# Kernel tuning notes

Hardware: AMD Instinct MI355X
Metric: run time of the kernel (lower is better)

## Reference

```python
import jax, jax.numpy as jnp
import numpy as np
from jax import lax

DN = ('NCDHW', 'OIDHW', 'NCDHW')

def conv3d(x, w, b=None):
    y = lax.conv_general_dilated(x, w, window_strides=(1, 1, 1), padding='SAME', dimension_numbers=DN)
    if b is not None:
        y = y + b[None, :, None, None, None]
    return y

def adaptive_conv(x, w):
    # x: [B,C,D,H,W]; w: [B,27,D,H,W] per-voxel 3x3x3 kernel weights
    B, C, D, H, W = x.shape
    xp = jnp.pad(x, ((0, 0), (0, 0), (1, 1), (1, 1), (1, 1)))
    out = jnp.zeros_like(x)
    idx = 0
    for i in range(3):
        for j in range(3):
            for k in range(3):
                out = out + xp[:, :, i:i + D, j:j + H, k:k + W] * w[:, idx][:, None]
                idx += 1
    return out

def setup_inputs() -> dict:
    key = jax.random.key(0)
    k1, k2, k3 = jax.random.split(key, 3)
    B, C, D, H, W = 1, 8, 128, 128, 128
    x = jax.random.normal(k1, (B, C, D, H, W), dtype=jnp.float32)
    w1 = jax.random.normal(k2, (8, 8, 3, 3, 3), dtype=jnp.float32) * 0.1
    b1 = jnp.zeros((8,), dtype=jnp.float32)
    w2 = jax.random.normal(k3, (27, 8, 3, 3, 3), dtype=jnp.float32) * 0.1
    return {"x": x, "w1": w1, "b1": b1, "w2": w2}

def reference(x, w1, b1, w2):
    # adaptive_block: per-voxel 27-tap weights from a small conv stack
    h = jax.nn.relu(conv3d(x, w1, b1))
    w = conv3d(h, w2)  # [B,27,D,H,W]
    # F.normalize(w, dim=1, p=1)
    n = jnp.sum(jnp.abs(w), axis=1, keepdims=True)
    w = w / jnp.maximum(n, 1e-12)
    out = x
    for _ in range(3):
        out = adaptive_conv(out, w)
    return out
```

## Files before the change

kernel.cpp:

```cpp
#include <hip/hip_runtime.h>
#include <hip/hip_bf16.h>

constexpr int HW2 = 16384;
constexpr int DHW = 2097152;

constexpr int PKG = 13;
constexpr int XT  = 130;

typedef short bf16x8 __attribute__((ext_vector_type(8)));
typedef float f32x4  __attribute__((ext_vector_type(4)));

__device__ inline unsigned short f2b(float f) {
  __hip_bfloat16 h = __float2bfloat16(f);
  return *(unsigned short*)&h;
}
__device__ inline float b2f(unsigned short u) {
  __hip_bfloat16 h = *(__hip_bfloat16*)&u;
  return __bfloat162float(h);
}

__global__ __launch_bounds__(256) void k_prep(
    const float* __restrict__ w1, const float* __restrict__ w2,
    unsigned short* __restrict__ Wpack2, unsigned short* __restrict__ Wpack1,
    float* __restrict__ g_ti, float* __restrict__ g_xi) {
  int i = blockIdx.x * 256 + threadIdx.x;
  if (i < 9216) {
    int j = i & 7;
    int lane = (i >> 3) & 63;
    int Mt = (i >> 9) & 1;
    int g2 = i >> 10;
    int s = g2 % 3, dx = g2 / 3;
    int oc = Mt * 16 + (lane & 15);
    int kr = s * 32 + (lane >> 4) * 8 + j;
    int ci = kr & 7, g = kr >> 3;
    float w = 0.f;
    if (oc < 27 && (g & 3) < 3) {
      int dzr = g >> 2, dyr = g & 3;
      w = w2[(oc * 8 + ci) * 27 + dzr * 9 + dyr * 3 + dx];
    }
    Wpack2[i] = f2b(w);
  }
  int jj = i - 9216;
  if (jj >= 0 && jj < 4608) {
    int j = jj & 7;
    int lane = (jj >> 3) & 63;
    int g2 = jj >> 9;
    int s = g2 % 3, dx = g2 / 3;
    int oc = lane & 15;
    int kr = s * 32 + (lane >> 4) * 8 + j;
    int ci = kr & 7, g = kr >> 3;
    float w = 0.f;
    if (oc < 8 && (g & 3) < 3) {
      int dzr = g >> 2, dyr = g & 3;
      w = w1[(oc * 8 + ci) * 27 + dzr * 9 + dyr * 3 + dx];
    }
    Wpack1[jj] = f2b(w);
  }
  int gg = i - 13824;
  if (gg >= 0 && gg < 32) {
    float* p = (gg < 8)  ? (g_ti - 8 + gg)
             : (gg < 16) ? (g_ti + (size_t)8 * DHW + (gg - 8))
             : (gg < 24) ? (g_xi - 8 + (gg - 16))
                         : (g_xi + (size_t)8 * DHW + (gg - 24));
    *p = 0.f;
  }
}

__global__ __launch_bounds__(256) void k_xpose(
    const float* __restrict__ x, unsigned short* __restrict__ xb,
    float* __restrict__ xi) {
  int idx = blockIdx.x * 256 + threadIdx.x;
  float f[8];
  unsigned v[4];
#pragma unroll
  for (int p = 0; p < 4; ++p) {
    f[2 * p]     = x[(size_t)(2 * p) * DHW + idx];
    f[2 * p + 1] = x[(size_t)(2 * p + 1) * DHW + idx];
    unsigned lo = f2b(f[2 * p]);
    unsigned hi = f2b(f[2 * p + 1]);
    v[p] = lo | (hi << 16);
  }
  ((uint4*)xb)[idx] = make_uint4(v[0], v[1], v[2], v[3]);
  float4* xo = (float4*)(xi + (size_t)idx * 8);
  xo[0] = make_float4(f[0], f[1], f[2], f[3]);
  xo[1] = make_float4(f[4], f[5], f[6], f[7]);
}

#define STAGE_ROWS2(srcp)                                                  \
  {                                                                        \
    if (tid < 154) {                                                       \
      if (tid < 130) {                                                     \
        dst[tid * PKG + 12] = make_uint4(0u, 0u, 0u, 0u);                  \
      } else {                                                             \
        int k = tid - 130;                                                 \
        int sl = k >> 1, xih = (k & 1) ? 129 : 0;                          \
        dst[xih * PKG + sl] = make_uint4(0u, 0u, 0u, 0u);                  \
      }                                                                    \
    }                                                                      \
    const int gg = tid >> 7;                                               \
    const int xi_ = (tid & 127) + 1;                                       \
    const int xg_ = xi_ - 1;                                               \
    uint4 sv[6];                                                           \
    bool vld[6];                                                           \
    _Pragma("unroll")                                                      \
    for (int it = 0; it < 6; ++it) {                                       \
      const int g = gg + it * 2;                                           \
      const int dz = g >> 2, ry = g & 3;                                   \
      const int z = z0 + dz - 1, y = y0 + ry - 1;                          \
      vld[it] = ((unsigned)z < 128u) & ((unsigned)y < 128u);               \
      const int zz = vld[it] ? z : z0, yy = vld[it] ? y : y0;              \
      sv[it] = (srcp)[(zz * 128 + yy) * 128 + xg_];                        \
    }                                                                      \
    _Pragma("unroll")                                                      \
    for (int it = 0; it < 6; ++it) {                                       \
      const int g = gg + it * 2;                                           \
      uint4 v = vld[it] ? sv[it] : make_uint4(0u, 0u, 0u, 0u);             \
      dst[xi_ * PKG + g] = v;                                              \
    }                                                                      \
  }

__global__ __launch_bounds__(256, 3) void k_conv1m(
    const unsigned short* __restrict__ xb,
    const unsigned short* __restrict__ Wpack1,
    const float* __restrict__ b1, unsigned short* __restrict__ hb) {
  __shared__ __align__(16) unsigned short T[XT * PKG * 8];
  const int tid  = threadIdx.x;
  const int lane = tid & 63;
  const int wv   = tid >> 6;
  const int logical = (blockIdx.x & 7) * 1024 + (blockIdx.x >> 3);
  const int z0 = logical >> 6;
  const int y0 = (logical & 63) * 2;

  bf16x8 wf[3][3];
  {
    const bf16x8* wp = (const bf16x8*)Wpack1;
#pragma unroll
    for (int dx = 0; dx < 3; ++dx)
#pragma unroll
      for (int s = 0; s < 3; ++s)
        wf[dx][s] = wp[(dx * 3 + s) * 64 + lane];
  }

  const uint4* src = (const uint4*)xb;
  uint4* dst = (uint4*)T;
  STAGE_ROWS2(src);
  __syncthreads();

  f32x4 acc[2][2];
#pragma unroll
  for (int r = 0; r < 2; ++r)
#pragma unroll
    for (int nt = 0; nt < 2; ++nt) acc[r][nt] = (f32x4){0.f, 0.f, 0.f, 0.f};

  const int n = lane & 15;
  const int q = lane >> 4;
  const int xbase = wv * 32 + n;

#pragma unroll
  for (int dx = 0; dx < 3; ++dx) {
#pragma unroll
    for (int s = 0; s < 3; ++s) {
      bf16x8 bfr[2][2];
#pragma unroll
      for (int r = 0; r < 2; ++r)
#pragma unroll
        for (int nt = 0; nt < 2; ++nt) {
          int off = ((xbase + nt * 16 + dx) * PKG + (s * 4 + q + r)) * 8;
          bfr[r][nt] = *(const bf16x8*)&T[off];
        }
#pragma unroll
      for (int r = 0; r < 2; ++r)
#pragma unroll
        for (int nt = 0; nt < 2; ++nt)
          acc[r][nt] = __builtin_amdgcn_mfma_f32_16x16x32_bf16(
              wf[dx][s], bfr[r][nt], acc[r][nt], 0, 0, 0);
    }
  }

  if (q < 2) {
#pragma unroll
    for (int r = 0; r < 2; ++r) {
      const int voxrow = (z0 * 128 + y0 + r) * 128;
#pragma unroll
      for (int nt = 0; nt < 2; ++nt) {
        const int vox = voxrow + wv * 32 + nt * 16 + n;
        ushort4 o;
        o.x = f2b(fmaxf(acc[r][nt][0] + b1[q * 4 + 0], 0.f));
        o.y = f2b(fmaxf(acc[r][nt][1] + b1[q * 4 + 1], 0.f));
        o.z = f2b(fmaxf(acc[r][nt][2] + b1[q * 4 + 2], 0.f));
        o.w = f2b(fmaxf(acc[r][nt][3] + b1[q * 4 + 3], 0.f));
        *(ushort4*)(hb + (size_t)vox * 8 + q * 4) = o;
      }
    }
  }
}

__global__ __launch_bounds__(256, 2) void k_conv2(
    const unsigned short* __restrict__ hb,
    const unsigned short* __restrict__ Wpack2,
    unsigned short* __restrict__ wn) {
  __shared__ __align__(16) unsigned short T[XT * PKG * 8];
  const int tid  = threadIdx.x;
  const int lane = tid & 63;
  const int wv   = tid >> 6;
  const int logical = (blockIdx.x & 7) * 1024 + (blockIdx.x >> 3);
  const int z0 = logical >> 6;
  const int y0 = (logical & 63) * 2;

  bf16x8 wf[3][3][2];
  {
    const bf16x8* wp = (const bf16x8*)Wpack2;
#pragma unroll
    for (int dx = 0; dx < 3; ++dx)
#pragma unroll
      for (int s = 0; s < 3; ++s)
#pragma unroll
        for (int mt = 0; mt < 2; ++mt)
          wf[dx][s][mt] = wp[((dx * 3 + s) * 2 + mt) * 64 + lane];
  }

  const uint4* src = (const uint4*)hb;
  uint4* dst = (uint4*)T;
  STAGE_ROWS2(src);
  __syncthreads();

  f32x4 acc[2][2][2];
#pragma unroll
  for (int r = 0; r < 2; ++r)
#pragma unroll
    for (int nt = 0; nt < 2; ++nt)
#pragma unroll
      for (int mt = 0; mt < 2; ++mt)
        acc[r][nt][mt] = (f32x4){0.f, 0.f, 0.f, 0.f};

  const int n = lane & 15;
  const int q = lane >> 4;
  const int xbase = wv * 32 + n;

#pragma unroll
  for (int dx = 0; dx < 3; ++dx) {
#pragma unroll
    for (int s = 0; s < 3; ++s) {
      bf16x8 bfr[2][2];
#pragma unroll
      for (int r = 0; r < 2; ++r)
#pragma unroll
        for (int nt = 0; nt < 2; ++nt) {
          int off = ((xbase + nt * 16 + dx) * PKG + (s * 4 + q + r)) * 8;
          bfr[r][nt] = *(const bf16x8*)&T[off];
        }
#pragma unroll
      for (int r = 0; r < 2; ++r)
#pragma unroll
        for (int mt = 0; mt < 2; ++mt)
#pragma unroll
          for (int nt = 0; nt < 2; ++nt)
            acc[r][nt][mt] = __builtin_amdgcn_mfma_f32_16x16x32_bf16(
                wf[dx][s][mt], bfr[r][nt], acc[r][nt][mt], 0, 0, 0);
    }
  }

#pragma unroll
  for (int r = 0; r < 2; ++r) {
    const int voxrow = (z0 * 128 + y0 + r) * 128;
#pragma unroll
    for (int nt = 0; nt < 2; ++nt) {
      float ns = 0.f;
#pragma unroll
      for (int rr = 0; rr < 4; ++rr) ns += fabsf(acc[r][nt][0][rr]);
#pragma unroll
      for (int rr = 0; rr < 4; ++rr) {
        int oc = 16 + q * 4 + rr;
        ns += (oc < 27) ? fabsf(acc[r][nt][1][rr]) : 0.f;
      }
      ns += __shfl_xor(ns, 16);
      ns += __shfl_xor(ns, 32);
      float sc = 1.f / fmaxf(ns, 1e-12f);
      const int vox = voxrow + wv * 32 + nt * 16 + n;
#pragma unroll
      for (int rr = 0; rr < 4; ++rr) {
        int oc = q * 4 + rr;
        wn[(size_t)oc * DHW + vox] = f2b(acc[r][nt][0][rr] * sc);
      }
#pragma unroll
      for (int rr = 0; rr < 4; ++rr) {
        int oc = 16 + q * 4 + rr;
        if (oc < 27)
          wn[(size_t)oc * DHW + vox] = f2b(acc[r][nt][1][rr] * sc);
      }
    }
  }
}

__device__ inline int swzb(int off) { return off ^ (((off >> 7) & 7) << 4); }

template <int FINAL>
__global__ __launch_bounds__(256, 2) void k_adapt4(
    const float* __restrict__ in, const unsigned short* __restrict__ wn,
    float* __restrict__ out) {
  __shared__ __align__(16) char S[16 * 4224];
  const int tid = threadIdx.x;
  const int logical = (blockIdx.x & 7) * 512 + (blockIdx.x >> 3);
  const int ty = logical & 63, tz = logical >> 6;
  const int y0 = ty * 2, z0 = tz * 2;

  const int wv = tid >> 6, lane = tid & 63;
  const int zl = wv >> 1, yl = wv & 1;
  const int zout = z0 + zl, yout = y0 + yl;
  const int xg = lane * 2;
  const int vox0 = (zout * 128 + yout) * 128 + xg;

  uint4 stg[16];
#pragma unroll
  for (int c = 0; c < 16; ++c) {
    const int zs = min(max(z0 - 1 + (c >> 2), 0), 127);
    const int ys = min(max(y0 - 1 + (c & 3), 0), 127);
    stg[c] = ((const uint4*)(in + (size_t)(zs * 128 + ys) * 1024))[tid];
  }

  unsigned wnv[27];
#pragma unroll
  for (int k = 0; k < 27; ++k)
    wnv[k] = *(const unsigned*)(wn + (size_t)k * DHW + vox0);

  {
    const int off = swzb(32 + tid * 16);
#pragma unroll
    for (int c = 0; c < 16; ++c)
      *(uint4*)(S + c * 4224 + off) = stg[c];
  }
  if (tid < 64) {
    const int row = tid >> 2, part = tid & 3;
    const int off = (part < 2) ? part * 16 : (4128 + (part - 2) * 16);
    *(uint4*)(S + row * 4224 + swzb(off)) = make_uint4(0u, 0u, 0u, 0u);
  }
  __syncthreads();

  int soff[4][2];
#pragma unroll
  for (int p = 0; p < 4; ++p)
#pragma unroll
    for (int h = 0; h < 2; ++h)
      soff[p][h] = swzb((xg + p) * 32 + h * 16);

  f32x4 a0A = (f32x4){0.f, 0.f, 0.f, 0.f};
  f32x4 a0B = (f32x4){0.f, 0.f, 0.f, 0.f};
  f32x4 a1A = (f32x4){0.f, 0.f, 0.f, 0.f};
  f32x4 a1B = (f32x4){0.f, 0.f, 0.f, 0.f};

#pragma unroll
  for (int g = 0; g < 9; ++g) {
    const int dzp = g / 3, dyp = g % 3;
    const char* R = S + ((zl + dzp) * 4 + (yl + dyp)) * 4224;
    f32x4 W[4][2];
#pragma unroll
    for (int p = 0; p < 4; ++p)
#pragma unroll
      for (int h = 0; h < 2; ++h)
        W[p][h] = *(const f32x4*)(R + soff[p][h]);
    const bool val = ((unsigned)(zout + dzp - 1) < 128u) &
                     ((unsigned)(yout + dyp - 1) < 128u);
#pragma unroll
    for (int dxi = 0; dxi < 3; ++dxi) {
      const unsigned u = wnv[g * 3 + dxi];
      const float wl = val ? b2f((unsigned short)(u & 0xffffu)) : 0.f;
      const float wh = val ? b2f((unsigned short)(u >> 16)) : 0.f;
#pragma unroll
      for (int c = 0; c < 4; ++c) {
        a0A[c] = fmaf(W[dxi][0][c], wl, a0A[c]);
        a0B[c] = fmaf(W[dxi][1][c], wl, a0B[c]);
        a1A[c] = fmaf(W[dxi + 1][0][c], wh, a1A[c]);
        a1B[c] = fmaf(W[dxi + 1][1][c], wh, a1B[c]);
      }
    }
  }

  if (FINAL) {
#pragma unroll
    for (int c = 0; c < 4; ++c) {
      *(float2*)(out + (size_t)c * DHW + vox0) = make_float2(a0A[c], a1A[c]);
      *(float2*)(out + (size_t)(c + 4) * DHW + vox0) =
          make_float2(a0B[c], a1B[c]);
    }
  } else {
    f32x4* op = (f32x4*)(out + (size_t)vox0 * 8);
    op[0] = a0A;
    op[1] = a0B;
    op[2] = a1A;
    op[3] = a1B;
  }
}

extern "C" void kernel_launch(void* const* d_in, const int* in_sizes, int n_in,
                              void* d_out, int out_size, void* d_ws, size_t ws_size,
                              hipStream_t stream) {
  const float* x  = (const float*)d_in[0];
  const float* w1 = (const float*)d_in[1];
  const float* b1 = (const float*)d_in[2];
  const float* w2 = (const float*)d_in[3];
  float* out = (float*)d_out;

  char* ws = (char*)d_ws;
  unsigned short* xb = (unsigned short*)ws;
  unsigned short* hb = (unsigned short*)(ws + (size_t)8 * DHW * 2);
  float* ti = (float*)(ws + 256);
  unsigned short* wn = (unsigned short*)(ws + (size_t)16 * DHW * 2 + 4096);
  float* xi = (float*)(ws + (size_t)16 * DHW * 2 + 4096 +
                       (size_t)27 * DHW * 2 + 8192);
  unsigned short* Wpack2 =
      (unsigned short*)((char*)xi + (size_t)8 * DHW * 4 + 16384);
  unsigned short* Wpack1 = Wpack2 + 9216;

  dim3 blk(256);
  k_prep<<<55, blk, 0, stream>>>(w1, w2, Wpack2, Wpack1, ti, xi);
  k_xpose<<<DHW / 256, blk, 0, stream>>>(x, xb, xi);
  k_conv1m<<<128 * 64, blk, 0, stream>>>(xb, Wpack1, b1, hb);
  k_conv2<<<128 * 64, blk, 0, stream>>>(hb, Wpack2, wn);
  k_adapt4<0><<<64 * 64, blk, 0, stream>>>(xi, wn, ti);
  k_adapt4<0><<<64 * 64, blk, 0, stream>>>(ti, wn, xi);
  k_adapt4<1><<<64 * 64, blk, 0, stream>>>(xi, wn, out);
}
```

Baseline: 353.3 us.

## Make adaptive conv kernel persistent over 8 y-tiles with register-prefetch pipelining

```diff
diff --git a/kernel.cpp b/kernel.cpp
--- a/kernel.cpp
+++ b/kernel.cpp
@@ -294,100 +294,149 @@
 
 __device__ inline int swzb(int off) { return off ^ (((off >> 7) & 7) << 4); }
 
+#define AD_ISSUE_X(ty_)                                                   \
+  {                                                                       \
+    const int ys0_ = 2 * (ty_) - 1;                                       \
+    _Pragma("unroll")                                                     \
+    for (int c = 0; c < 16; ++c) {                                        \
+      const int ys_ = min(max(ys0_ + (c & 3), 0), 127);                   \
+      stg[c] =                                                            \
+          ((const uint4*)(in + (size_t)(zs4[c >> 2] * 128 + ys_) * 1024)) \
+              [tid];                                                      \
+    }                                                                     \
+  }
+
+#define AD_ISSUE_WN(W_, ty_)                                              \
+  {                                                                       \
+    const int vox_ = (zrow + 2 * (ty_) + yl) * 128 + xg;                  \
+    _Pragma("unroll")                                                     \
+    for (int k2 = 0; k2 < 27; ++k2)                                       \
+      W_[k2] = *(const unsigned*)(wn + (size_t)k2 * DHW + vox_);          \
+  }
+
+#define AD_DSW()                                                          \
+  {                                                                       \
+    _Pragma("unroll")                                                     \
+    for (int c = 0; c < 16; ++c)                                          \
+      *(uint4*)(S + c * 4224 + woff) = stg[c];                            \
+  }
+
+#define AD_COMPUTE(W_, ty_)                                               \
+  {                                                                       \
+    const int yout_ = 2 * (ty_) + yl;                                     \
+    const int vox0_ = (zrow + yout_) * 128 + xg;                          \
+    f32x4 a0A = (f32x4){0.f, 0.f, 0.f, 0.f};                              \
+    f32x4 a0B = (f32x4){0.f, 0.f, 0.f, 0.f};                              \
+    f32x4 a1A = (f32x4){0.f, 0.f, 0.f, 0.f};                              \
+    f32x4 a1B = (f32x4){0.f, 0.f, 0.f, 0.f};                              \
+    _Pragma("unroll")                                                     \
+    for (int g = 0; g < 9; ++g) {                                         \
+      const int dzp_ = g / 3, dyp_ = g % 3;                               \
+      const char* R_ = S + ((zl + dzp_) * 4 + (yl + dyp_)) * 4224;        \
+      f32x4 W4[4][2];                                                     \
+      _Pragma("unroll")                                                   \
+      for (int p = 0; p < 4; ++p)                                         \
+        _Pragma("unroll")                                                 \
+        for (int h = 0; h < 2; ++h)                                       \
+          W4[p][h] = *(const f32x4*)(R_ + soff[p][h]);                    \
+      const bool val_ =                                                   \
+          zok[dzp_] & ((unsigned)(yout_ + dyp_ - 1) < 128u);              \
+      _Pragma("unroll")                                                   \
+      for (int dxi = 0; dxi < 3; ++dxi) {                                 \
+        const unsigned u_ = W_[g * 3 + dxi];                              \
+        const float wl_ =                                                 \
+            val_ ? b2f((unsigned short)(u_ & 0xffffu)) : 0.f;             \
+        const float wh_ = val_ ? b2f((unsigned short)(u_ >> 16)) : 0.f;   \
+        _Pragma("unroll")                                                 \
+        for (int c = 0; c < 4; ++c) {                                     \
+          a0A[c] = fmaf(W4[dxi][0][c], wl_, a0A[c]);                      \
+          a0B[c] = fmaf(W4[dxi][1][c], wl_, a0B[c]);                      \
+          a1A[c] = fmaf(W4[dxi + 1][0][c], wh_, a1A[c]);                  \
+          a1B[c] = fmaf(W4[dxi + 1][1][c], wh_, a1B[c]);                  \
+        }                                                                 \
+      }                                                                   \
+    }                                                                     \
+    if (FINAL) {                                                          \
+      _Pragma("unroll")                                                   \
+      for (int c = 0; c < 4; ++c) {                                       \
+        *(float2*)(out + (size_t)c * DHW + vox0_) =                       \
+            make_float2(a0A[c], a1A[c]);                                  \
+        *(float2*)(out + (size_t)(c + 4) * DHW + vox0_) =                 \
+            make_float2(a0B[c], a1B[c]);                                  \
+      }                                                                   \
+    } else {                                                              \
+      f32x4* op_ = (f32x4*)(out + (size_t)vox0_ * 8);                     \
+      op_[0] = a0A;                                                       \
+      op_[1] = a0B;                                                       \
+      op_[2] = a1A;                                                       \
+      op_[3] = a1B;                                                       \
+    }                                                                     \
+  }
+
 template <int FINAL>
-__global__ __launch_bounds__(256, 2) void k_adapt4(
+__global__ __launch_bounds__(256, 2) void k_adapt5(
     const float* __restrict__ in, const unsigned short* __restrict__ wn,
     float* __restrict__ out) {
   __shared__ __align__(16) char S[16 * 4224];
   const int tid = threadIdx.x;
-  const int logical = (blockIdx.x & 7) * 512 + (blockIdx.x >> 3);
-  const int ty = logical & 63, tz = logical >> 6;
-  const int y0 = ty * 2, z0 = tz * 2;
-
   const int wv = tid >> 6, lane = tid & 63;
   const int zl = wv >> 1, yl = wv & 1;
-  const int zout = z0 + zl, yout = y0 + yl;
   const int xg = lane * 2;
-  const int vox0 = (zout * 128 + yout) * 128 + xg;
-
-  uint4 stg[16];
-#pragma unroll
-  for (int c = 0; c < 16; ++c) {
-    const int zs = min(max(z0 - 1 + (c >> 2), 0), 127);
-    const int ys = min(max(y0 - 1 + (c & 3), 0), 127);
-    stg[c] = ((const uint4*)(in + (size_t)(zs * 128 + ys) * 1024))[tid];
-  }
-
-  unsigned wnv[27];
-#pragma unroll
-  for (int k = 0; k < 27; ++k)
-    wnv[k] = *(const unsigned*)(wn + (size_t)k * DHW + vox0);
-
-  {
-    const int off = swzb(32 + tid * 16);
-#pragma unroll
-    for (int c = 0; c < 16; ++c)
-      *(uint4*)(S + c * 4224 + off) = stg[c];
-  }
+
+  const int logical_b = ((blockIdx.x & 7) << 6) + (blockIdx.x >> 3);
+  const int tz = logical_b >> 3;
+  const int ty0 = (logical_b & 7) * 8;
+
+  int zs4[4];
+#pragma unroll
+  for (int d = 0; d < 4; ++d) zs4[d] = min(max(2 * tz - 1 + d, 0), 127);
+  bool zok[3];
+#pragma unroll
+  for (int d = 0; d < 3; ++d)
+    zok[d] = (unsigned)(2 * tz + zl + d - 1) < 128u;
+  const int zrow = (2 * tz + zl) * 128;
+
+  const int woff = swzb(32 + tid * 16);
+  int soff[4][2];
+#pragma unroll
+  for (int p = 0; p < 4; ++p)
+#pragma unroll
+    for (int h = 0; h < 2; ++h)
+      soff[p][h] = swzb((xg + p) * 32 + h * 16);
+
   if (tid < 64) {
     const int row = tid >> 2, part = tid & 3;
     const int off = (part < 2) ? part * 16 : (4128 + (part - 2) * 16);
-    *(uint4*)(S + row * 4224 + swzb(off)) = make_uint4(0u, 0u, 0u, 0u);
-  }
+    *(uint4*)(S + row * 4224 + off) = make_uint4(0u, 0u, 0u, 0u);
+  }
+
+  uint4 stg[16];
+  unsigned wnA[27], wnB[27];
+
+  AD_ISSUE_X(ty0);
+  AD_ISSUE_WN(wnA, ty0);
+  AD_DSW();
   __syncthreads();
 
-  int soff[4][2];
-#pragma unroll
-  for (int p = 0; p < 4; ++p)
-#pragma unroll
-    for (int h = 0; h < 2; ++h)
-      soff[p][h] = swzb((xg + p) * 32 + h * 16);
-
-  f32x4 a0A = (f32x4){0.f, 0.f, 0.f, 0.f};
-  f32x4 a0B = (f32x4){0.f, 0.f, 0.f, 0.f};
-  f32x4 a1A = (f32x4){0.f, 0.f, 0.f, 0.f};
-  f32x4 a1B = (f32x4){0.f, 0.f, 0.f, 0.f};
-
-#pragma unroll
-  for (int g = 0; g < 9; ++g) {
-    const int dzp = g / 3, dyp = g % 3;
-    const char* R = S + ((zl + dzp) * 4 + (yl + dyp)) * 4224;
-    f32x4 W[4][2];
-#pragma unroll
-    for (int p = 0; p < 4; ++p)
-#pragma unroll
-      for (int h = 0; h < 2; ++h)
-        W[p][h] = *(const f32x4*)(R + soff[p][h]);
-    const bool val = ((unsigned)(zout + dzp - 1) < 128u) &
-                     ((unsigned)(yout + dyp - 1) < 128u);
-#pragma unroll
-    for (int dxi = 0; dxi < 3; ++dxi) {
-      const unsigned u = wnv[g * 3 + dxi];
-      const float wl = val ? b2f((unsigned short)(u & 0xffffu)) : 0.f;
-      const float wh = val ? b2f((unsigned short)(u >> 16)) : 0.f;
-#pragma unroll
-      for (int c = 0; c < 4; ++c) {
-        a0A[c] = fmaf(W[dxi][0][c], wl, a0A[c]);
-        a0B[c] = fmaf(W[dxi][1][c], wl, a0B[c]);
-        a1A[c] = fmaf(W[dxi + 1][0][c], wh, a1A[c]);
-        a1B[c] = fmaf(W[dxi + 1][1][c], wh, a1B[c]);
-      }
-    }
-  }
-
-  if (FINAL) {
-#pragma unroll
-    for (int c = 0; c < 4; ++c) {
-      *(float2*)(out + (size_t)c * DHW + vox0) = make_float2(a0A[c], a1A[c]);
-      *(float2*)(out + (size_t)(c + 4) * DHW + vox0) =
-          make_float2(a0B[c], a1B[c]);
-    }
-  } else {
-    f32x4* op = (f32x4*)(out + (size_t)vox0 * 8);
-    op[0] = a0A;
-    op[1] = a0B;
-    op[2] = a1A;
-    op[3] = a1B;
+#pragma unroll 1
+  for (int k = 0; k < 4; ++k) {
+    const int tyA = ty0 + 2 * k;
+    const int tyB = tyA + 1;
+    const int tyC = (k < 3) ? (tyA + 2) : tyB;
+
+    AD_ISSUE_X(tyB);
+    AD_ISSUE_WN(wnB, tyB);
+    AD_COMPUTE(wnA, tyA);
+    __syncthreads();
+    AD_DSW();
+    __syncthreads();
+
+    AD_ISSUE_X(tyC);
+    AD_ISSUE_WN(wnA, tyC);
+    AD_COMPUTE(wnB, tyB);
+    __syncthreads();
+    AD_DSW();
+    __syncthreads();
   }
 }
 
@@ -416,7 +465,7 @@
   k_xpose<<<DHW / 256, blk, 0, stream>>>(x, xb, xi);
   k_conv1m<<<128 * 64, blk, 0, stream>>>(xb, Wpack1, b1, hb);
   k_conv2<<<128 * 64, blk, 0, stream>>>(hb, Wpack2, wn);
-  k_adapt4<0><<<64 * 64, blk, 0, stream>>>(xi, wn, ti);
-  k_adapt4<0><<<64 * 64, blk, 0, stream>>>(ti, wn, xi);
-  k_adapt4<1><<<64 * 64, blk, 0, stream>>>(xi, wn, out);
-}
+  k_adapt5<0><<<512, blk, 0, stream>>>(xi, wn, ti);
+  k_adapt5<0><<<512, blk, 0, stream>>>(ti, wn, xi);
+  k_adapt5<1><<<512, blk, 0, stream>>>(xi, wn, out);
+}
```

Measured after the change: 820.5 us. 2.32x slower.

## Use one voxel per thread with 512-thread blocks in adaptive conv

Applied to the files above, without the earlier changes.

```diff
diff --git a/kernel.cpp b/kernel.cpp
--- a/kernel.cpp
+++ b/kernel.cpp
@@ -292,10 +292,12 @@
   }
 }
 
-__device__ inline int swzb(int off) { return off ^ (((off >> 7) & 7) << 4); }
+__device__ inline int swzb(int off) {
+  return off ^ ((((off >> 7) ^ (off >> 10)) & 7) << 4);
+}
 
 template <int FINAL>
-__global__ __launch_bounds__(256, 2) void k_adapt4(
+__global__ __launch_bounds__(512, 2) void k_adapt6(
     const float* __restrict__ in, const unsigned short* __restrict__ wn,
     float* __restrict__ out) {
   __shared__ __align__(16) char S[16 * 4224];
@@ -304,30 +306,34 @@
   const int ty = logical & 63, tz = logical >> 6;
   const int y0 = ty * 2, z0 = tz * 2;
 
-  const int wv = tid >> 6, lane = tid & 63;
-  const int zl = wv >> 1, yl = wv & 1;
+  const int r = tid >> 7;
+  const int zl = r >> 1, yl = r & 1;
+  const int x = tid & 127;
   const int zout = z0 + zl, yout = y0 + yl;
-  const int xg = lane * 2;
-  const int vox0 = (zout * 128 + yout) * 128 + xg;
-
-  uint4 stg[16];
-#pragma unroll
-  for (int c = 0; c < 16; ++c) {
-    const int zs = min(max(z0 - 1 + (c >> 2), 0), 127);
-    const int ys = min(max(y0 - 1 + (c & 3), 0), 127);
-    stg[c] = ((const uint4*)(in + (size_t)(zs * 128 + ys) * 1024))[tid];
-  }
-
-  unsigned wnv[27];
+  const int vox = (zout * 128 + yout) * 128 + x;
+
+  const int sh = tid >> 8;
+  const int spos = tid & 255;
+
+  uint4 stg[8];
+#pragma unroll
+  for (int c = 0; c < 8; ++c) {
+    const int row = sh * 8 + c;
+    const int zs = min(max(z0 - 1 + (row >> 2), 0), 127);
+    const int ys = min(max(y0 - 1 + (row & 3), 0), 127);
+    stg[c] = ((const uint4*)(in + (size_t)(zs * 128 + ys) * 1024))[spos];
+  }
+
+  unsigned short wnv[27];
 #pragma unroll
   for (int k = 0; k < 27; ++k)
-    wnv[k] = *(const unsigned*)(wn + (size_t)k * DHW + vox0);
+    wnv[k] = wn[(size_t)k * DHW + vox];
 
   {
-    const int off = swzb(32 + tid * 16);
-#pragma unroll
-    for (int c = 0; c < 16; ++c)
-      *(uint4*)(S + c * 4224 + off) = stg[c];
+    const int woff = swzb(32 + spos * 16);
+#pragma unroll
+    for (int c = 0; c < 8; ++c)
+      *(uint4*)(S + (sh * 8 + c) * 4224 + woff) = stg[c];
   }
   if (tid < 64) {
     const int row = tid >> 2, part = tid & 3;
@@ -336,58 +342,57 @@
   }
   __syncthreads();
 
-  int soff[4][2];
-#pragma unroll
-  for (int p = 0; p < 4; ++p)
+  int soff[3][2];
+#pragma unroll
+  for (int p = 0; p < 3; ++p)
 #pragma unroll
     for (int h = 0; h < 2; ++h)
-      soff[p][h] = swzb((xg + p) * 32 + h * 16);
-
-  f32x4 a0A = (f32x4){0.f, 0.f, 0.f, 0.f};
-  f32x4 a0B = (f32x4){0.f, 0.f, 0.f, 0.f};
-  f32x4 a1A = (f32x4){0.f, 0.f, 0.f, 0.f};
-  f32x4 a1B = (f32x4){0.f, 0.f, 0.f, 0.f};
-
+      soff[p][h] = swzb((x + p) * 32 + h * 16);
+
+  bool zok[3], yok[3];
+#pragma unroll
+  for (int d = 0; d < 3; ++d) {
+    zok[d] = (unsigned)(zout + d - 1) < 128u;
+    yok[d] = (unsigned)(yout + d - 1) < 128u;
+  }
+
+  f32x4 aA = (f32x4){0.f, 0.f, 0.f, 0.f};
+  f32x4 aB = (f32x4){0.f, 0.f, 0.f, 0.f};
+
+  __builtin_amdgcn_s_setprio(1);
 #pragma unroll
   for (int g = 0; g < 9; ++g) {
     const int dzp = g / 3, dyp = g % 3;
     const char* R = S + ((zl + dzp) * 4 + (yl + dyp)) * 4224;
-    f32x4 W[4][2];
-#pragma unroll
-    for (int p = 0; p < 4; ++p)
+    f32x4 W[3][2];
+#pragma unroll
+    for (int p = 0; p < 3; ++p)
 #pragma unroll
       for (int h = 0; h < 2; ++h)
         W[p][h] = *(const f32x4*)(R + soff[p][h]);
-    const bool val = ((unsigned)(zout + dzp - 1) < 128u) &
-                     ((unsigned)(yout + dyp - 1) < 128u);
+    const bool val = zok[dzp] & yok[dyp];
 #pragma unroll
     for (int dxi = 0; dxi < 3; ++dxi) {
-      const unsigned u = wnv[g * 3 + dxi];
-      const float wl = val ? b2f((unsigned short)(u & 0xffffu)) : 0.f;
-      const float wh = val ? b2f((unsigned short)(u >> 16)) : 0.f;
+      const float w = val ? b2f(wnv[g * 3 + dxi]) : 0.f;
 #pragma unroll
       for (int c = 0; c < 4; ++c) {
-        a0A[c] = fmaf(W[dxi][0][c], wl, a0A[c]);
-        a0B[c] = fmaf(W[dxi][1][c], wl, a0B[c]);
-        a1A[c] = fmaf(W[dxi + 1][0][c], wh, a1A[c]);
-        a1B[c] = fmaf(W[dxi + 1][1][c], wh, a1B[c]);
+        aA[c] = fmaf(W[dxi][0][c], w, aA[c]);
+        aB[c] = fmaf(W[dxi][1][c], w, aB[c]);
       }
     }
   }
+  __builtin_amdgcn_s_setprio(0);
 
   if (FINAL) {
 #pragma unroll
     for (int c = 0; c < 4; ++c) {
-      *(float2*)(out + (size_t)c * DHW + vox0) = make_float2(a0A[c], a1A[c]);
-      *(float2*)(out + (size_t)(c + 4) * DHW + vox0) =
-          make_float2(a0B[c], a1B[c]);
+      out[(size_t)c * DHW + vox] = aA[c];
+      out[(size_t)(c + 4) * DHW + vox] = aB[c];
     }
   } else {
-    f32x4* op = (f32x4*)(out + (size_t)vox0 * 8);
-    op[0] = a0A;
-    op[1] = a0B;
-    op[2] = a1A;
-    op[3] = a1B;
+    f32x4* op = (f32x4*)(out + (size_t)vox * 8);
+    op[0] = aA;
+    op[1] = aB;
   }
 }
 
@@ -412,11 +417,12 @@
   unsigned short* Wpack1 = Wpack2 + 9216;
 
   dim3 blk(256);
+  dim3 blk512(512);
   k_prep<<<55, blk, 0, stream>>>(w1, w2, Wpack2, Wpack1, ti, xi);
   k_xpose<<<DHW / 256, blk, 0, stream>>>(x, xb, xi);
   k_conv1m<<<128 * 64, blk, 0, stream>>>(xb, Wpack1, b1, hb);
   k_conv2<<<128 * 64, blk, 0, stream>>>(hb, Wpack2, wn);
-  k_adapt4<0><<<64 * 64, blk, 0, stream>>>(xi, wn, ti);
-  k_adapt4<0><<<64 * 64, blk, 0, stream>>>(ti, wn, xi);
-  k_adapt4<1><<<64 * 64, blk, 0, stream>>>(xi, wn, out);
-}
+  k_adapt6<0><<<64 * 64, blk512, 0, stream>>>(xi, wn, ti);
+  k_adapt6<0><<<64 * 64, blk512, 0, stream>>>(ti, wn, xi);
+  k_adapt6<1><<<64 * 64, blk512, 0, stream>>>(xi, wn, out);
+}
```

After: 359.6 us. Within noise of the previous version (+1.8%).

## Retile adaptive conv to 4x4x64 blocks with two y-outputs per thread

Applied to the files above, without the earlier changes.

```diff
diff --git a/kernel.cpp b/kernel.cpp
--- a/kernel.cpp
+++ b/kernel.cpp
@@ -292,102 +292,142 @@
   }
 }
 
-__device__ inline int swzb(int off) { return off ^ (((off >> 7) & 7) << 4); }
+constexpr int APITCH = 2112;
+__device__ inline int swz7(int off) { return off ^ (((off >> 7) & 7) << 4); }
 
 template <int FINAL>
-__global__ __launch_bounds__(256, 2) void k_adapt4(
+__global__ __launch_bounds__(256, 2) void k_adapt7(
     const float* __restrict__ in, const unsigned short* __restrict__ wn,
     float* __restrict__ out) {
-  __shared__ __align__(16) char S[16 * 4224];
+  __shared__ __align__(16) char S[36 * APITCH];
   const int tid = threadIdx.x;
-  const int logical = (blockIdx.x & 7) * 512 + (blockIdx.x >> 3);
-  const int ty = logical & 63, tz = logical >> 6;
-  const int y0 = ty * 2, z0 = tz * 2;
-
-  const int wv = tid >> 6, lane = tid & 63;
-  const int zl = wv >> 1, yl = wv & 1;
-  const int zout = z0 + zl, yout = y0 + yl;
-  const int xg = lane * 2;
-  const int vox0 = (zout * 128 + yout) * 128 + xg;
-
-  uint4 stg[16];
-#pragma unroll
-  for (int c = 0; c < 16; ++c) {
-    const int zs = min(max(z0 - 1 + (c >> 2), 0), 127);
-    const int ys = min(max(y0 - 1 + (c & 3), 0), 127);
-    stg[c] = ((const uint4*)(in + (size_t)(zs * 128 + ys) * 1024))[tid];
-  }
-
-  unsigned wnv[27];
-#pragma unroll
-  for (int k = 0; k < 27; ++k)
-    wnv[k] = *(const unsigned*)(wn + (size_t)k * DHW + vox0);
-
-  {
-    const int off = swzb(32 + tid * 16);
-#pragma unroll
-    for (int c = 0; c < 16; ++c)
-      *(uint4*)(S + c * 4224 + off) = stg[c];
-  }
-  if (tid < 64) {
-    const int row = tid >> 2, part = tid & 3;
-    const int off = (part < 2) ? part * 16 : (4128 + (part - 2) * 16);
-    *(uint4*)(S + row * 4224 + swzb(off)) = make_uint4(0u, 0u, 0u, 0u);
+  const int logical = (blockIdx.x & 7) * 256 + (blockIdx.x >> 3);
+  const int xh  = logical & 1;
+  const int typ = (logical >> 1) & 31;
+  const int tzp = logical >> 6;
+  const int x0 = xh * 64, y0 = typ * 4, z0 = tzp * 4;
+
+  const int xp = tid & 31;
+  const int yp = (tid >> 5) & 1;
+  const int zo = tid >> 6;
+
+  uint4 stg[19];
+#pragma unroll
+  for (int i = 0; i < 19; ++i) {
+    const int c = tid + 256 * i;
+    if (c < 4752) {
+      const int r = c / 132;
+      const int k = c - r * 132;
+      const int r6 = r / 6;
+      const int zs = min(max(z0 - 1 + r6, 0), 127);
+      const int ys = min(max(y0 - 1 + (r - r6 * 6), 0), 127);
+      const float* gp = in + (size_t)(zs * 128 + ys) * 1024 +
+                        (ptrdiff_t)((x0 - 1) * 8 + k * 4);
+      stg[i] = *(const uint4*)gp;
+    }
+  }
+#pragma unroll
+  for (int i = 0; i < 19; ++i) {
+    const int c = tid + 256 * i;
+    if (c < 4752) {
+      const int r = c / 132;
+      const int k = c - r * 132;
+      const bool halo = xh ? (k >= 130) : (k < 2);
+      const uint4 v = halo ? make_uint4(0u, 0u, 0u, 0u) : stg[i];
+      *(uint4*)(S + r * APITCH + swz7(k * 16)) = v;
+    }
   }
   __syncthreads();
 
+  const int Y = y0 + 2 * yp;
+  const int Z = z0 + zo;
+  bool zok[3];
+#pragma unroll
+  for (int d = 0; d < 3; ++d) zok[d] = (unsigned)(Z + d - 1) < 128u;
+  bool yok[2][3];
+#pragma unroll
+  for (int oy = 0; oy < 2; ++oy)
+#pragma unroll
+    for (int d = 0; d < 3; ++d)
+      yok[oy][d] = (unsigned)(Y + oy + d - 1) < 128u;
+
   int soff[4][2];
 #pragma unroll
-  for (int p = 0; p < 4; ++p)
+  for (int j = 0; j < 4; ++j)
 #pragma unroll
     for (int h = 0; h < 2; ++h)
-      soff[p][h] = swzb((xg + p) * 32 + h * 16);
-
-  f32x4 a0A = (f32x4){0.f, 0.f, 0.f, 0.f};
-  f32x4 a0B = (f32x4){0.f, 0.f, 0.f, 0.f};
-  f32x4 a1A = (f32x4){0.f, 0.f, 0.f, 0.f};
-  f32x4 a1B = (f32x4){0.f, 0.f, 0.f, 0.f};
-
-#pragma unroll
-  for (int g = 0; g < 9; ++g) {
-    const int dzp = g / 3, dyp = g % 3;
-    const char* R = S + ((zl + dzp) * 4 + (yl + dyp)) * 4224;
-    f32x4 W[4][2];
-#pragma unroll
-    for (int p = 0; p < 4; ++p)
+      soff[j][h] = swz7((2 * xp + j) * 32 + h * 16);
+
+  const size_t voxp0 = (size_t)(Z * 128 + Y) * 128 + x0 + 2 * xp;
+
+  f32x4 acc[2][2][2];
+#pragma unroll
+  for (int oy = 0; oy < 2; ++oy)
+#pragma unroll
+    for (int ox = 0; ox < 2; ++ox)
 #pragma unroll
       for (int h = 0; h < 2; ++h)
-        W[p][h] = *(const f32x4*)(R + soff[p][h]);
-    const bool val = ((unsigned)(zout + dzp - 1) < 128u) &
-                     ((unsigned)(yout + dyp - 1) < 128u);
-#pragma unroll
-    for (int dxi = 0; dxi < 3; ++dxi) {
-      const unsigned u = wnv[g * 3 + dxi];
-      const float wl = val ? b2f((unsigned short)(u & 0xffffu)) : 0.f;
-      const float wh = val ? b2f((unsigned short)(u >> 16)) : 0.f;
-#pragma unroll
-      for (int c = 0; c < 4; ++c) {
-        a0A[c] = fmaf(W[dxi][0][c], wl, a0A[c]);
-        a0B[c] = fmaf(W[dxi][1][c], wl, a0B[c]);
-        a1A[c] = fmaf(W[dxi + 1][0][c], wh, a1A[c]);
-        a1B[c] = fmaf(W[dxi + 1][1][c], wh, a1B[c]);
+        acc[oy][ox][h] = (f32x4){0.f, 0.f, 0.f, 0.f};
+
+#pragma unroll
+  for (int dz = 0; dz < 3; ++dz) {
+#pragma unroll
+    for (int yr = 0; yr < 4; ++yr) {
+      const char* R = S + ((zo + dz) * 6 + 2 * yp + yr) * APITCH;
+      f32x4 W[4][2];
+#pragma unroll
+      for (int j = 0; j < 4; ++j)
+#pragma unroll
+        for (int h = 0; h < 2; ++h)
+          W[j][h] = *(const f32x4*)(R + soff[j][h]);
+#pragma unroll
+      for (int oy = 0; oy < 2; ++oy) {
+        const int dy = yr - oy;
+        if (dy >= 0 && dy < 3) {
+          const bool val = zok[dz] & yok[oy][dy];
+          const size_t voxp = voxp0 + (size_t)oy * 128;
+#pragma unroll
+          for (int dxi = 0; dxi < 3; ++dxi) {
+            const unsigned u = *(const unsigned*)(
+                wn + (size_t)(dz * 9 + dy * 3 + dxi) * DHW + voxp);
+            const float w0 = val ? b2f((unsigned short)(u & 0xffffu)) : 0.f;
+            const float w1 = val ? b2f((unsigned short)(u >> 16)) : 0.f;
+#pragma unroll
+            for (int h = 0; h < 2; ++h)
+#pragma unroll
+              for (int c = 0; c < 4; ++c) {
+                acc[oy][0][h][c] = fmaf(W[dxi][h][c], w0, acc[oy][0][h][c]);
+                acc[oy][1][h][c] =
+                    fmaf(W[dxi + 1][h][c], w1, acc[oy][1][h][c]);
+              }
+          }
+        }
       }
     }
   }
 
   if (FINAL) {
 #pragma unroll
-    for (int c = 0; c < 4; ++c) {
-      *(float2*)(out + (size_t)c * DHW + vox0) = make_float2(a0A[c], a1A[c]);
-      *(float2*)(out + (size_t)(c + 4) * DHW + vox0) =
-          make_float2(a0B[c], a1B[c]);
+    for (int oy = 0; oy < 2; ++oy) {
+      const size_t voxp = voxp0 + (size_t)oy * 128;
+#pragma unroll
+      for (int h = 0; h < 2; ++h)
+#pragma unroll
+        for (int c = 0; c < 4; ++c) {
+          float2 o = make_float2(acc[oy][0][h][c], acc[oy][1][h][c]);
+          *(float2*)(out + (size_t)(h * 4 + c) * DHW + voxp) = o;
+        }
     }
   } else {
-    f32x4* op = (f32x4*)(out + (size_t)vox0 * 8);
-    op[0] = a0A;
-    op[1] = a0B;
-    op[2] = a1A;
-    op[3] = a1B;
+#pragma unroll
+    for (int oy = 0; oy < 2; ++oy) {
+      const size_t voxp = voxp0 + (size_t)oy * 128;
+      f32x4* op = (f32x4*)(out + voxp * 8);
+      op[0] = acc[oy][0][0];
+      op[1] = acc[oy][0][1];
+      op[2] = acc[oy][1][0];
+      op[3] = acc[oy][1][1];
+    }
   }
 }
 
@@ -416,7 +456,7 @@
   k_xpose<<<DHW / 256, blk, 0, stream>>>(x, xb, xi);
   k_conv1m<<<128 * 64, blk, 0, stream>>>(xb, Wpack1, b1, hb);
   k_conv2<<<128 * 64, blk, 0, stream>>>(hb, Wpack2, wn);
-  k_adapt4<0><<<64 * 64, blk, 0, stream>>>(xi, wn, ti);
-  k_adapt4<0><<<64 * 64, blk, 0, stream>>>(ti, wn, xi);
-  k_adapt4<1><<<64 * 64, blk, 0, stream>>>(xi, wn, out);
-}
+  k_adapt7<0><<<2048, blk, 0, stream>>>(xi, wn, ti);
+  k_adapt7<0><<<2048, blk, 0, stream>>>(ti, wn, xi);
+  k_adapt7<1><<<2048, blk, 0, stream>>>(xi, wn, out);
+}
```

Measured after the change: 781.6 us. 2.21x slower.
